# Kernel tuning notes

Hardware: AMD Instinct MI355X
Metric: run time of the kernel (lower is better)

Reference implementation:

```python
import jax, jax.numpy as jnp
import numpy as np

B, SEQ, DIM, HEADS = 2, 2048, 512, 8
HD = DIM // HEADS
RANK, DFF = 128, 1024
TAU_MEM, TAU_ADAPT, SLOPE, EPS = 0.99, 0.95, 25.0, 1e-6
THRESH, ADAPT_STRENGTH = 0.5, 0.1
TREE_LEVELS = int(np.log2(SEQ))  # 11


def rmsnorm(x, w, eps=EPS):
    return x * jax.lax.rsqrt(jnp.mean(x * x, axis=-1, keepdims=True) + eps) * w


def rope_cos_sin(seq, hd):
    inv = 1.0 / (10000.0 ** (jnp.arange(0, hd, 2, dtype=jnp.float32) / hd))
    f = jnp.arange(seq, dtype=jnp.float32)[:, None] * inv[None, :]  # [S, hd/2]
    emb = jnp.concatenate([f, f], axis=-1)  # [S, hd]
    return jnp.cos(emb), jnp.sin(emb)


def apply_rope(x, cos, sin):
    # x: [B, H, S, hd]; rotate-half formulation
    x1, x2 = jnp.split(x, 2, axis=-1)
    return x * cos + jnp.concatenate([-x2, x1], axis=-1) * sin


def setup_inputs() -> dict:
    key = jax.random.key(0)
    ks = jax.random.split(key, 12)
    w = lambda k, shape, fan: (jax.random.normal(k, shape, jnp.float32) / np.sqrt(fan))
    return {
        "x": jax.random.normal(ks[0], (B, SEQ, DIM), jnp.float32),
        "norm_w": jnp.ones((DIM,), jnp.float32),
        "wq": w(ks[1], (DIM, DIM), DIM),
        "wk": w(ks[2], (DIM, DIM), DIM),
        "wv": w(ks[3], (DIM, DIM), DIM),
        "wo": w(ks[4], (DIM, DIM), DIM),
        "lat_w": w(ks[5], (SEQ, SEQ), SEQ),
        "bt": jnp.full((DIM,), THRESH, jnp.float32),
        "as_w": jnp.full((DIM,), ADAPT_STRENGTH, jnp.float32),
        "gate_w": w(ks[6], (DIM, DIM), DIM),
        "tnorm1_w": jnp.ones((DIM,), jnp.float32),
        "tnorm2_w": jnp.ones((DIM,), jnp.float32),
        "ffn_norm_w": jnp.ones((DIM,), jnp.float32),
        "u_w": w(ks[7], (DIM, RANK), DIM),
        "v_w": w(ks[8], (RANK, 2 * DFF), RANK),
        "down_w": w(ks[9], (DFF, DIM), DFF),
    }


def reference(x, norm_w, wq, wk, wv, wo, lat_w, bt, as_w, gate_w,
              tnorm1_w, tnorm2_w, ffn_norm_w, u_w, v_w, down_w):
    Bx, S, D = x.shape
    # --- pre-norm + QKV projections (base_proj) ---
    h = rmsnorm(x, norm_w)
    q = (h @ wq.T).reshape(Bx, S, HEADS, HD).transpose(0, 2, 1, 3)  # [B,H,S,hd]
    k = (h @ wk.T).reshape(Bx, S, HEADS, HD).transpose(0, 2, 1, 3)
    v = (h @ wv.T).reshape(Bx, S, HEADS, HD).transpose(0, 2, 1, 3)
    # --- RoPE ---
    cos, sin = rope_cos_sin(S, HD)
    q = apply_rope(q, cos, sin)
    k = apply_rope(k, cos, sin)
    # --- causal self-attention ---
    scores = jnp.einsum("bhqd,bhkd->bhqk", q, k) / np.sqrt(HD)
    causal = jnp.tril(jnp.ones((S, S), bool))
    scores = jnp.where(causal, scores, jnp.float32(-1e9))
    attn = jnp.einsum("bhqk,bhkd->bhqd", jax.nn.softmax(scores, axis=-1), v)
    attn = attn.transpose(0, 2, 1, 3).reshape(Bx, S, D) @ wo.T
    # --- causal lateral mixing across sequence ---
    mixed = jnp.einsum("ts,bsd->btd", jnp.tril(lat_w), attn)
    # --- ALIF spiking recurrence over the sequence (soft surrogate spike) ---
    def alif_step(carry, i_t):
        vmem, ad = carry
        vmem = TAU_MEM * vmem + i_t
        th = bt + as_w * ad
        spike = jax.nn.sigmoid(SLOPE * (vmem - th))
        vmem = vmem - spike * th          # soft reset
        ad = TAU_ADAPT * ad + spike        # threshold adaptation
        return (vmem, ad), spike
    init = (jnp.zeros((Bx, D), x.dtype), jnp.zeros((Bx, D), x.dtype))
    _, spikes = jax.lax.scan(alif_step, init, mixed.transpose(1, 0, 2))
    spikes = spikes.transpose(1, 0, 2)  # [B,S,D]
    # --- fused addadd residual ---
    h2 = x + mixed + spikes
    # --- binary-tree cell recursion to a root summary ---
    s = h2
    for _ in range(TREE_LEVELS):
        raw = s[:, 0::2, :] + s[:, 1::2, :]         # pairwise sums (raw_sums)
        res = 0.5 * raw                              # residual / prev_s surrogate
        n = rmsnorm(raw, tnorm1_w)
        g = jax.nn.sigmoid(n @ gate_w.T)
        s = rmsnorm(g * n + (1.0 - g) * res, tnorm2_w)
    h3 = h2 + s[:, 0:1, :]  # broadcast root back over the sequence
    # --- low-rank SwiGLU FFN ---
    hn = rmsnorm(h3, ffn_norm_w)
    up = (hn @ u_w) @ v_w                 # [B,S,2*DFF]
    a, b = jnp.split(up, 2, axis=-1)
    ffn = (jax.nn.silu(a) * b) @ down_w   # [B,S,D]
    return h3 + ffn
```

## Files before the change

kernel.cpp:

```cpp
#include <hip/hip_runtime.h>
#include <math.h>

#define BB 2
#define SS 2048
#define DD 512
#define HH 8
#define HDD 64
#define RANKK 128
#define DFFF 1024

typedef short bf16x8 __attribute__((ext_vector_type(8)));
typedef float f32x4 __attribute__((ext_vector_type(4)));

__device__ __forceinline__ short f2b(float f) {
  union { float f; unsigned u; } v; v.f = f;
  unsigned r = v.u + 0x7FFF + ((v.u >> 16) & 1);
  return (short)(r >> 16);
}
__device__ __forceinline__ float b2f(short s) {
  union { unsigned u; float f; } v; v.u = ((unsigned)(unsigned short)s) << 16;
  return v.f;
}

__device__ __forceinline__ void gll16(const void* g, void* l) {
  __builtin_amdgcn_global_load_lds(
      (const __attribute__((address_space(1))) unsigned int*)g,
      (__attribute__((address_space(3))) unsigned int*)l, 16, 0, 0);
}

__device__ __forceinline__ float wsum(float v) {
#pragma unroll
  for (int off = 32; off > 0; off >>= 1) v += __shfl_xor(v, off, 64);
  return v;
}

__global__ void splitw4(const float* __restrict__ w0, const float* __restrict__ w1,
                        const float* __restrict__ w2, const float* __restrict__ w3,
                        short* h0, short* l0_, short* h1, short* l1_,
                        short* h2_, short* l2_, short* h3_, short* l3_) {
  const int z = blockIdx.z;
  const float* in = (z == 0) ? w0 : (z == 1) ? w1 : (z == 2) ? w2 : w3;
  short* hi = (z == 0) ? h0 : (z == 1) ? h1 : (z == 2) ? h2_ : h3_;
  short* lo = (z == 0) ? l0_ : (z == 1) ? l1_ : (z == 2) ? l2_ : l3_;
  int i = (blockIdx.x * 256 + threadIdx.x) * 4;
  if (i >= DD * DD) return;
  float4 v = *(const float4*)(in + i);
  short4 h4, l4;
  h4.x = f2b(v.x); l4.x = f2b(v.x - b2f(h4.x));
  h4.y = f2b(v.y); l4.y = f2b(v.y - b2f(h4.y));
  h4.z = f2b(v.z); l4.z = f2b(v.z - b2f(h4.z));
  h4.w = f2b(v.w); l4.w = f2b(v.w - b2f(h4.w));
  *(short4*)(hi + i) = h4;
  *(short4*)(lo + i) = l4;
}

__global__ void splitlat(const float* __restrict__ lat, short* __restrict__ hi,
                         short* __restrict__ lo) {
  int i = (blockIdx.x * 256 + threadIdx.x) * 4;
  int r = i >> 11;
  int c = i & 2047;
  float4 v = *(const float4*)(lat + i);
  if (c + 0 > r) v.x = 0.0f;
  if (c + 1 > r) v.y = 0.0f;
  if (c + 2 > r) v.z = 0.0f;
  if (c + 3 > r) v.w = 0.0f;
  short4 h4, l4;
  h4.x = f2b(v.x); l4.x = f2b(v.x - b2f(h4.x));
  h4.y = f2b(v.y); l4.y = f2b(v.y - b2f(h4.y));
  h4.z = f2b(v.z); l4.z = f2b(v.z - b2f(h4.z));
  h4.w = f2b(v.w); l4.w = f2b(v.w - b2f(h4.w));
  *(short4*)(hi + i) = h4;
  *(short4*)(lo + i) = l4;
}

__global__ void cvtb(const float* __restrict__ in, short* __restrict__ out, int n) {
  int i = (blockIdx.x * 256 + threadIdx.x) * 4;
  if (i >= n) return;
  float4 v = *(const float4*)(in + i);
  short4 o; o.x = f2b(v.x); o.y = f2b(v.y); o.z = f2b(v.z); o.w = f2b(v.w);
  *(short4*)(out + i) = o;
}

__global__ void sum2(const float* __restrict__ a, const float* __restrict__ bq,
                     float* __restrict__ o) {
  int i = (blockIdx.x * 256 + threadIdx.x) * 4;
  float4 va = *(const float4*)(a + i);
  float4 vb = *(const float4*)(bq + i);
  float4 vo = {va.x + vb.x, va.y + vb.y, va.z + vb.z, va.w + vb.w};
  *(float4*)(o + i) = vo;
}

__global__ void transp_cvt(const float* __restrict__ in, short* __restrict__ out,
                           int R, int C) {
  __shared__ float t[32][33];
  int c0 = blockIdx.x * 32, r0 = blockIdx.y * 32;
#pragma unroll
  for (int i = 0; i < 4; i++) {
    int idx = threadIdx.x + i * 256;
    int r = idx >> 5, c = idx & 31;
    t[r][c] = in[(size_t)(r0 + r) * C + c0 + c];
  }
  __syncthreads();
#pragma unroll
  for (int i = 0; i < 4; i++) {
    int idx = threadIdx.x + i * 256;
    int cc = idx >> 5, rr = idx & 31;
    out[(size_t)(c0 + cc) * R + r0 + rr] = f2b(t[rr][cc]);
  }
}

__global__ void rmsnorm_hl(const float* __restrict__ x, const float* __restrict__ w,
                           short* __restrict__ oh, short* __restrict__ ol, int rows) {
  int wid = blockIdx.x * 4 + (threadIdx.x >> 6);
  int lane = threadIdx.x & 63;
  if (wid >= rows) return;
  const float* xp = x + (size_t)wid * DD + lane * 8;
  float4 a = *(const float4*)xp;
  float4 b = *(const float4*)(xp + 4);
  float ss = a.x*a.x + a.y*a.y + a.z*a.z + a.w*a.w
           + b.x*b.x + b.y*b.y + b.z*b.z + b.w*b.w;
  ss = wsum(ss);
  float r = rsqrtf(ss * (1.0f / DD) + 1e-6f);
  const float* wp = w + lane * 8;
  float4 wa = *(const float4*)wp, wb = *(const float4*)(wp + 4);
  float o8[8] = {a.x*r*wa.x, a.y*r*wa.y, a.z*r*wa.z, a.w*r*wa.w,
                 b.x*r*wb.x, b.y*r*wb.y, b.z*r*wb.z, b.w*r*wb.w};
  short hv[8], lv[8];
#pragma unroll
  for (int i = 0; i < 8; i++) { hv[i] = f2b(o8[i]); lv[i] = f2b(o8[i] - b2f(hv[i])); }
  short* op = oh + (size_t)wid * DD + lane * 8;
  short* lp = ol + (size_t)wid * DD + lane * 8;
  *(short4*)op = make_short4(hv[0], hv[1], hv[2], hv[3]);
  *(short4*)(op + 4) = make_short4(hv[4], hv[5], hv[6], hv[7]);
  *(short4*)lp = make_short4(lv[0], lv[1], lv[2], lv[3]);
  *(short4*)(lp + 4) = make_short4(lv[4], lv[5], lv[6], lv[7]);
}

template <bool SPL, int OM, bool ROPE>
__global__ __launch_bounds__(256) void ggemm(const short* __restrict__ Ah_g,
                                             const short* __restrict__ Al_g,
                                             const short* __restrict__ Bh_g,
                                             const short* __restrict__ Bl_g,
                                             const float* __restrict__ ADD,
                                             void* __restrict__ C, void* __restrict__ C2,
                                             int M, int N, int K) {
  __shared__ short Ahs[128 * 32];
  __shared__ short Bhs[128 * 32];
  __shared__ short Als[SPL ? 128 * 32 : 8];
  __shared__ short Bls[SPL ? 128 * 32 : 8];
  const int tid = threadIdx.x, l = tid & 63, w = tid >> 6;
  const int wr = (w >> 1) * 64, wc = (w & 1) * 64;
  const int bm = blockIdx.y * 128, bn = blockIdx.x * 128;
  f32x4 acc[4][4] = {};
  for (int k0 = 0; k0 < K; k0 += 32) {
#pragma unroll
    for (int p = 0; p < 2; p++) {
      int row = p * 64 + (tid >> 2), g = tid & 3;
      int swz = (g ^ ((row >> 1) & 3)) * 8;
      gll16(Ah_g + (size_t)(bm + row) * K + k0 + swz, Ahs + p * 2048 + tid * 8);
      gll16(Bh_g + (size_t)(bn + row) * K + k0 + swz, Bhs + p * 2048 + tid * 8);
      if (SPL) {
        gll16(Al_g + (size_t)(bm + row) * K + k0 + swz, Als + p * 2048 + tid * 8);
        gll16(Bl_g + (size_t)(bn + row) * K + k0 + swz, Bls + p * 2048 + tid * 8);
      }
    }
    __syncthreads();
    bf16x8 ah[4], bh[4], al[4], bl[4];
#pragma unroll
    for (int m = 0; m < 4; m++) {
      int r = wr + m * 16 + (l & 15);
      int go = (((l >> 4) ^ ((r >> 1) & 3)) << 3);
      ah[m] = *(const bf16x8*)(Ahs + r * 32 + go);
      if (SPL) al[m] = *(const bf16x8*)(Als + r * 32 + go);
    }
#pragma unroll
    for (int n = 0; n < 4; n++) {
      int r = wc + n * 16 + (l & 15);
      int go = (((l >> 4) ^ ((r >> 1) & 3)) << 3);
      bh[n] = *(const bf16x8*)(Bhs + r * 32 + go);
      if (SPL) bl[n] = *(const bf16x8*)(Bls + r * 32 + go);
    }
#pragma unroll
    for (int m = 0; m < 4; m++)
#pragma unroll
      for (int n = 0; n < 4; n++) {
        acc[m][n] = __builtin_amdgcn_mfma_f32_16x16x32_bf16(ah[m], bh[n], acc[m][n], 0, 0, 0);
        if (SPL) {
          acc[m][n] = __builtin_amdgcn_mfma_f32_16x16x32_bf16(ah[m], bl[n], acc[m][n], 0, 0, 0);
          acc[m][n] = __builtin_amdgcn_mfma_f32_16x16x32_bf16(al[m], bh[n], acc[m][n], 0, 0, 0);
        }
      }
    __syncthreads();
  }
  const int ll = l & 15, lg4 = (l >> 4) * 4;
  if (ROPE) {
#pragma unroll
    for (int m = 0; m < 4; m++)
#pragma unroll
      for (int n = 0; n < 2; n++) {
        int i_ = n * 16 + ll;
        float inv = exp2f(-(float)i_ * (13.287712379549449f / 32.0f));
#pragma unroll
        for (int j = 0; j < 4; j++) {
          int gm = bm + wr + m * 16 + lg4 + j;
          int s = gm & (SS - 1);
          float ang = (float)s * inv;
          float sn, cs;
          sincosf(ang, &sn, &cs);
          float v1 = acc[m][n][j], v2 = acc[m][n + 2][j];
          acc[m][n][j]     = v1 * cs - v2 * sn;
          acc[m][n + 2][j] = v2 * cs + v1 * sn;
        }
      }
  }
#pragma unroll
  for (int m = 0; m < 4; m++)
#pragma unroll
    for (int n = 0; n < 4; n++) {
      int gn = bn + wc + n * 16 + ll;
#pragma unroll
      for (int j = 0; j < 4; j++) {
        int gm = bm + wr + m * 16 + lg4 + j;
        if (gm >= M || gn >= N) continue;
        float v = acc[m][n][j];
        if (OM == 0) {
          ((float*)C)[(size_t)gm * N + gn] = v;
        } else if (OM == 1) {
          ((short*)C)[(size_t)gm * N + gn] = f2b(v);
        } else if (OM == 6) {
          size_t off = (size_t)gm * N + gn;
          ((float*)C)[off] = v + ADD[off];
        } else {
          short hi = f2b(v);
          short lo = f2b(v - b2f(hi));
          int b = gm >> 11, s = gm & (SS - 1);
          int hh2 = gn >> 6, d = gn & 63;
          size_t off;
          if (OM == 2)      off = (((size_t)(b * HH + hh2)) * SS + s) * 64 + d;
          else if (OM == 3) off = (((size_t)(b * HH + hh2)) * 64 + d) * SS + s;
          else              off = ((size_t)(b * DD) + gn) * SS + s;
          ((short*)C)[off] = hi;
          ((short*)C2)[off] = lo;
        }
      }
    }
}

__global__ __launch_bounds__(256) void qkv_g(const short* __restrict__ Ah_g,
                                             const short* __restrict__ Al_g,
                                             const short* __restrict__ wh0, const short* __restrict__ wl0,
                                             const short* __restrict__ wh1, const short* __restrict__ wl1,
                                             const short* __restrict__ wh2, const short* __restrict__ wl2,
                                             short* __restrict__ c0h, short* __restrict__ c0l,
                                             short* __restrict__ c1h, short* __restrict__ c1l,
                                             short* __restrict__ c2h, short* __restrict__ c2l) {
  const int z = blockIdx.z;
  const short* Bh_g = (z == 0) ? wh0 : (z == 1) ? wh1 : wh2;
  const short* Bl_g = (z == 0) ? wl0 : (z == 1) ? wl1 : wl2;
  short* Ch = (z == 0) ? c0h : (z == 1) ? c1h : c2h;
  short* Cl = (z == 0) ? c0l : (z == 1) ? c1l : c2l;
  const int K = DD;
  __shared__ short Ahs[128 * 32];
  __shared__ short Bhs[128 * 32];
  __shared__ short Als[128 * 32];
  __shared__ short Bls[128 * 32];
  const int tid = threadIdx.x, l = tid & 63, w = tid >> 6;
  const int wr = (w >> 1) * 64, wc = (w & 1) * 64;
  const int bm = blockIdx.y * 128, bn = blockIdx.x * 128;
  f32x4 acc[4][4] = {};
  for (int k0 = 0; k0 < K; k0 += 32) {
#pragma unroll
    for (int p = 0; p < 2; p++) {
      int row = p * 64 + (tid >> 2), g = tid & 3;
      int swz = (g ^ ((row >> 1) & 3)) * 8;
      gll16(Ah_g + (size_t)(bm + row) * K + k0 + swz, Ahs + p * 2048 + tid * 8);
      gll16(Bh_g + (size_t)(bn + row) * K + k0 + swz, Bhs + p * 2048 + tid * 8);
      gll16(Al_g + (size_t)(bm + row) * K + k0 + swz, Als + p * 2048 + tid * 8);
      gll16(Bl_g + (size_t)(bn + row) * K + k0 + swz, Bls + p * 2048 + tid * 8);
    }
    __syncthreads();
    bf16x8 ah[4], bh[4], al[4], bl[4];
#pragma unroll
    for (int m = 0; m < 4; m++) {
      int r = wr + m * 16 + (l & 15);
      int go = (((l >> 4) ^ ((r >> 1) & 3)) << 3);
      ah[m] = *(const bf16x8*)(Ahs + r * 32 + go);
      al[m] = *(const bf16x8*)(Als + r * 32 + go);
    }
#pragma unroll
    for (int n = 0; n < 4; n++) {
      int r = wc + n * 16 + (l & 15);
      int go = (((l >> 4) ^ ((r >> 1) & 3)) << 3);
      bh[n] = *(const bf16x8*)(Bhs + r * 32 + go);
      bl[n] = *(const bf16x8*)(Bls + r * 32 + go);
    }
#pragma unroll
    for (int m = 0; m < 4; m++)
#pragma unroll
      for (int n = 0; n < 4; n++) {
        acc[m][n] = __builtin_amdgcn_mfma_f32_16x16x32_bf16(ah[m], bh[n], acc[m][n], 0, 0, 0);
        acc[m][n] = __builtin_amdgcn_mfma_f32_16x16x32_bf16(ah[m], bl[n], acc[m][n], 0, 0, 0);
        acc[m][n] = __builtin_amdgcn_mfma_f32_16x16x32_bf16(al[m], bh[n], acc[m][n], 0, 0, 0);
      }
    __syncthreads();
  }
  const int ll = l & 15, lg4 = (l >> 4) * 4;
  if (z < 2) {
#pragma unroll
    for (int m = 0; m < 4; m++)
#pragma unroll
      for (int n = 0; n < 2; n++) {
        int i_ = n * 16 + ll;
        float inv = exp2f(-(float)i_ * (13.287712379549449f / 32.0f));
#pragma unroll
        for (int j = 0; j < 4; j++) {
          int gm = bm + wr + m * 16 + lg4 + j;
          int s = gm & (SS - 1);
          float ang = (float)s * inv;
          float sn, cs;
          sincosf(ang, &sn, &cs);
          float v1 = acc[m][n][j], v2 = acc[m][n + 2][j];
          acc[m][n][j]     = v1 * cs - v2 * sn;
          acc[m][n + 2][j] = v2 * cs + v1 * sn;
        }
      }
  }
#pragma unroll
  for (int m = 0; m < 4; m++)
#pragma unroll
    for (int n = 0; n < 4; n++) {
      int gn = bn + wc + n * 16 + ll;
#pragma unroll
      for (int j = 0; j < 4; j++) {
        int gm = bm + wr + m * 16 + lg4 + j;
        float v = acc[m][n][j];
        short hi = f2b(v);
        short lo = f2b(v - b2f(hi));
        int b = gm >> 11, s = gm & (SS - 1);
        int hh2 = gn >> 6, d = gn & 63;
        size_t off = (z < 2) ? ((((size_t)(b * HH + hh2)) * SS + s) * 64 + d)
                             : ((((size_t)(b * HH + hh2)) * 64 + d) * SS + s);
        Ch[off] = hi;
        Cl[off] = lo;
      }
    }
}

__global__ __launch_bounds__(256) void lat_g(const short* __restrict__ lath,
                                             const short* __restrict__ latl,
                                             const short* __restrict__ bTh,
                                             const short* __restrict__ bTl,
                                             float* __restrict__ P0,
                                             float* __restrict__ P1) {
  const int zb = blockIdx.z >> 1;
  const int half = blockIdx.z & 1;
  bTh += (size_t)zb * DD * SS;
  bTl += (size_t)zb * DD * SS;
  float* Cc = (half == 0 ? P0 : P1) + (size_t)zb * DD * SS;
  __shared__ short Ah[128 * 32];
  __shared__ short Al[128 * 32];
  __shared__ short Bh[128 * 32];
  __shared__ short Bl[128 * 32];
  const int tid = threadIdx.x, l = tid & 63, w = tid >> 6;
  const int wr = (w >> 1) * 64, wc = (w & 1) * 64;
  const int bm = blockIdx.y * 128, bn = blockIdx.x * 128;
  const int T = blockIdx.y + 1;
  const int h0 = (T + 1) >> 1;
  const int kbeg = (half == 0) ? 0 : h0 * 128;
  const int kend = (half == 0) ? h0 * 128 : T * 128;
  f32x4 acc[4][4] = {};
  const int ll = l & 15, lg4 = (l >> 4) * 4;
  for (int k0 = kbeg; k0 < kend; k0 += 32) {
#pragma unroll
    for (int p = 0; p < 2; p++) {
      int row = p * 64 + (tid >> 2), g = tid & 3;
      int swz = (g ^ ((row >> 1) & 3)) * 8;
      gll16(bTh + (size_t)(bn + row) * SS + k0 + swz, Bh + p * 2048 + tid * 8);
      gll16(bTl + (size_t)(bn + row) * SS + k0 + swz, Bl + p * 2048 + tid * 8);
      gll16(lath + (size_t)(bm + row) * SS + k0 + swz, Ah + p * 2048 + tid * 8);
      gll16(latl + (size_t)(bm + row) * SS + k0 + swz, Al + p * 2048 + tid * 8);
    }
    __syncthreads();
    bf16x8 ah[4], bh[4], al[4], bl[4];
#pragma unroll
    for (int m = 0; m < 4; m++) {
      int r = wr + m * 16 + (l & 15);
      int go = (((l >> 4) ^ ((r >> 1) & 3)) << 3);
      ah[m] = *(const bf16x8*)(Ah + r * 32 + go);
      al[m] = *(const bf16x8*)(Al + r * 32 + go);
    }
#pragma unroll
    for (int n = 0; n < 4; n++) {
      int r = wc + n * 16 + (l & 15);
      int go = (((l >> 4) ^ ((r >> 1) & 3)) << 3);
      bh[n] = *(const bf16x8*)(Bh + r * 32 + go);
      bl[n] = *(const bf16x8*)(Bl + r * 32 + go);
    }
#pragma unroll
    for (int m = 0; m < 4; m++)
#pragma unroll
      for (int n = 0; n < 4; n++) {
        acc[m][n] = __builtin_amdgcn_mfma_f32_16x16x32_bf16(ah[m], bh[n], acc[m][n], 0, 0, 0);
        acc[m][n] = __builtin_amdgcn_mfma_f32_16x16x32_bf16(ah[m], bl[n], acc[m][n], 0, 0, 0);
        acc[m][n] = __builtin_amdgcn_mfma_f32_16x16x32_bf16(al[m], bh[n], acc[m][n], 0, 0, 0);
      }
    __syncthreads();
  }
#pragma unroll
  for (int m = 0; m < 4; m++)
#pragma unroll
    for (int n = 0; n < 4; n++) {
      int gn = bn + wc + n * 16 + ll;
#pragma unroll
      for (int j = 0; j < 4; j++) {
        int gm = bm + wr + m * 16 + lg4 + j;
        size_t off = ((size_t)((gm >> 5) * 512 + gn)) * 32 + ((gm + gn) & 31);
        Cc[off] = acc[m][n][j];
      }
    }
}

__global__ __launch_bounds__(256) void attn_g(const short* __restrict__ qh,
                                              const short* __restrict__ ql,
                                              const short* __restrict__ kh,
                                              const short* __restrict__ kl,
                                              const short* __restrict__ vh,
                                              const short* __restrict__ vl,
                                              short* __restrict__ aho,
                                              short* __restrict__ alo) {
  const int h = blockIdx.y, b = blockIdx.z;
  const int qt = (b == 0) ? (int)blockIdx.x : 31 - (int)blockIdx.x;
  const int q0 = qt * 64;
  const int tid = threadIdx.x, w = tid >> 6, l = tid & 63;
  const int lg = l >> 4, ll = l & 15;
  __shared__ short Kh[64 * 64], Kl[64 * 64];
  __shared__ short Vh[64 * 64], Vl[64 * 64];
  __shared__ short Ph[64 * 64];
  const size_t bh = (size_t)(b * HH + h);

  const int qr = q0 + w * 16 + ll;
  const short* qbh = qh + (bh * SS + qr) * 64;
  const short* qbl = ql + (bh * SS + qr) * 64;
  bf16x8 qfh[2], qfl[2];
#pragma unroll
  for (int ks = 0; ks < 2; ks++) {
    qfh[ks] = *(const bf16x8*)(qbh + (ks * 4 + lg) * 8);
    qfl[ks] = *(const bf16x8*)(qbl + (ks * 4 + lg) * 8);
  }

  f32x4 o[4] = {};
  float mrow[4] = {-1e30f, -1e30f, -1e30f, -1e30f};
  float lsum[4] = {};
  const int qrow0 = q0 + w * 16 + lg * 4;
  const int ntiles = qt + 1;

  for (int kt = 0; kt < ntiles; kt++) {
#pragma unroll
    for (int p = 0; p < 2; p++) {
      int row = p * 32 + (tid >> 3), g = tid & 7;
      int sw = ((g ^ (row & 7)) << 3);
      size_t krow = (bh * SS + kt * 64 + row) * 64;
      size_t vrow = (bh * 64 + row) * SS + kt * 64;
      gll16(kh + krow + sw, Kh + p * 2048 + tid * 8);
      gll16(kl + krow + sw, Kl + p * 2048 + tid * 8);
      gll16(vh + vrow + sw, Vh + p * 2048 + tid * 8);
      gll16(vl + vrow + sw, Vl + p * 2048 + tid * 8);
    }
    __syncthreads();

    f32x4 sv[4] = {};
#pragma unroll
    for (int nf = 0; nf < 4; nf++) {
      int r = nf * 16 + ll;
#pragma unroll
      for (int ks = 0; ks < 2; ks++) {
        int g = (ks * 4 + lg) ^ (r & 7);
        bf16x8 khf = *(const bf16x8*)(Kh + r * 64 + g * 8);
        bf16x8 klf = *(const bf16x8*)(Kl + r * 64 + g * 8);
        sv[nf] = __builtin_amdgcn_mfma_f32_16x16x32_bf16(qfh[ks], khf, sv[nf], 0, 0, 0);
        sv[nf] = __builtin_amdgcn_mfma_f32_16x16x32_bf16(qfh[ks], klf, sv[nf], 0, 0, 0);
        sv[nf] = __builtin_amdgcn_mfma_f32_16x16x32_bf16(qfl[ks], khf, sv[nf], 0, 0, 0);
      }
    }
#pragma unroll
    for (int nf = 0; nf < 4; nf++) {
      int kpos = kt * 64 + nf * 16 + ll;
#pragma unroll
      for (int j = 0; j < 4; j++) {
        float v = sv[nf][j] * 0.125f;
        sv[nf][j] = (kpos > qrow0 + j) ? -1e30f : v;
      }
    }
    float cf[4];
#pragma unroll
    for (int j = 0; j < 4; j++) {
      float r = fmaxf(fmaxf(sv[0][j], sv[1][j]), fmaxf(sv[2][j], sv[3][j]));
      r = fmaxf(r, __shfl_xor(r, 1)); r = fmaxf(r, __shfl_xor(r, 2));
      r = fmaxf(r, __shfl_xor(r, 4)); r = fmaxf(r, __shfl_xor(r, 8));
      float mn = fmaxf(mrow[j], r);
      cf[j] = __expf(mrow[j] - mn);
      mrow[j] = mn;
    }
    float ps[4] = {};
#pragma unroll
    for (int nf = 0; nf < 4; nf++)
#pragma unroll
      for (int j = 0; j < 4; j++) {
        float p = __expf(sv[nf][j] - mrow[j]);
        sv[nf][j] = p;
        ps[j] += p;
      }
#pragma unroll
    for (int j = 0; j < 4; j++) {
      float r = ps[j];
      r += __shfl_xor(r, 1); r += __shfl_xor(r, 2);
      r += __shfl_xor(r, 4); r += __shfl_xor(r, 8);
      lsum[j] = lsum[j] * cf[j] + r;
    }
#pragma unroll
    for (int nf = 0; nf < 4; nf++)
#pragma unroll
      for (int j = 0; j < 4; j++) o[nf][j] *= cf[j];
#pragma unroll
    for (int nf = 0; nf < 4; nf++)
#pragma unroll
      for (int j = 0; j < 4; j++) {
        int rowP = w * 16 + lg * 4 + j;
        int col = nf * 16 + ll;
        int off = rowP * 64 + (((col >> 3) ^ (rowP & 7)) << 3) + (col & 7);
        Ph[off] = f2b(sv[nf][j]);
      }
    __syncthreads();
    bf16x8 pfh[2];
    {
      int rowA = w * 16 + ll;
#pragma unroll
      for (int ks = 0; ks < 2; ks++) {
        int g = (ks * 4 + lg) ^ (rowA & 7);
        pfh[ks] = *(const bf16x8*)(Ph + rowA * 64 + g * 8);
      }
    }
#pragma unroll
    for (int nf = 0; nf < 4; nf++) {
      int r = nf * 16 + ll;
#pragma unroll
      for (int ks = 0; ks < 2; ks++) {
        int g = (ks * 4 + lg) ^ (r & 7);
        bf16x8 vhf = *(const bf16x8*)(Vh + r * 64 + g * 8);
        bf16x8 vlf = *(const bf16x8*)(Vl + r * 64 + g * 8);
        o[nf] = __builtin_amdgcn_mfma_f32_16x16x32_bf16(pfh[ks], vhf, o[nf], 0, 0, 0);
        o[nf] = __builtin_amdgcn_mfma_f32_16x16x32_bf16(pfh[ks], vlf, o[nf], 0, 0, 0);
      }
    }
    __syncthreads();
  }
  float inv[4];
#pragma unroll
  for (int j = 0; j < 4; j++) inv[j] = 1.0f / lsum[j];
#pragma unroll
  for (int nf = 0; nf < 4; nf++)
#pragma unroll
    for (int j = 0; j < 4; j++) {
      float v = o[nf][j] * inv[j];
      short hi = f2b(v);
      size_t off = ((size_t)(b * SS + qrow0 + j)) * DD + h * HDD + nf * 16 + ll;
      aho[off] = hi;
      alo[off] = f2b(v - b2f(hi));
    }
}

#define ACH 32
__global__ __launch_bounds__(64) void tsa_alif8(const float* __restrict__ mixedS,
                                                const float* __restrict__ bt,
                                                const float* __restrict__ asw,
                                                float* __restrict__ spikesS) {
  __shared__ float lds[2][ACH * 64];
  const int t = threadIdx.x;
  const int tid = blockIdx.x * 64 + t;
  const int b = tid >> 9, d = tid & 511;
  const int d0 = d & ~63;
  const float btd = bt[d], asd = asw[d];
  const float C = 36.06737602222409f;
  const float bt36 = btd * C, as36 = asd * C;
  const float bt99 = 0.99f * btd, as99 = 0.99f * asd;
  const size_t bbase = (size_t)b * DD * SS;
  const float* mp = mixedS + bbase;
  float* sp = spikesS + bbase;
  {
    const float* g0 = mp + (size_t)d0 * 32;
#pragma unroll
    for (int i = 0; i < 8; i++) gll16(g0 + i * 256 + t * 4, &lds[0][i * 256 + t * 4]);
  }
  float vR = 0.0f, ad = 0.0f;
  for (int c = 0; c < SS / ACH; c++) {
    const int cur = c & 1;
    __syncthreads();
    if (c + 1 < SS / ACH) {
      const float* gq = mp + ((size_t)((c + 1) * 512 + d0)) * 32;
#pragma unroll
      for (int i = 0; i < 8; i++) gll16(gq + i * 256 + t * 4, &lds[cur ^ 1][i * 256 + t * 4]);
    }
    float m[ACH];
#pragma unroll
    for (int j = 0; j < ACH; j++) m[j] = lds[cur][t * 32 + ((j + t) & 31)];
    vR += m[0];
    float sO[ACH];
#pragma unroll
    for (int j = 0; j < ACH; j++) {
      float thC = fmaf(ad, as36, bt36);
      float th99 = fmaf(ad, as99, bt99);
      float arg = fmaf(vR, -C, thC);
      float e = exp2f(arg);
      float s = __builtin_amdgcn_rcpf(1.0f + e);
      sO[j] = s;
      float pre = (j + 1 < ACH) ? fmaf(0.99f, vR, m[j + 1]) : (0.99f * vR);
      vR = fmaf(-th99, s, pre);
      ad = fmaf(0.95f, ad, s);
    }
#pragma unroll
    for (int j = 0; j < ACH; j++) lds[cur][t * 32 + ((j + t) & 31)] = sO[j];
    __syncthreads();
    float* so = sp + ((size_t)(c * 512 + d0)) * 32;
#pragma unroll
    for (int i = 0; i < 8; i++) {
      float4 v4 = *(const float4*)&lds[cur][i * 256 + t * 4];
      *(float4*)(so + i * 256 + t * 4) = v4;
    }
  }
}

__global__ __launch_bounds__(256) void fuse_h2(const float* __restrict__ x,
                                               const float* __restrict__ mixedS,
                                               const float* __restrict__ spikesS,
                                               float* __restrict__ h2) {
  const int s0 = blockIdx.x * 64, d0 = blockIdx.y * 64, b = blockIdx.z;
  __shared__ float t[64][65];
  const int dl = threadIdx.x >> 2;
  const int grp = threadIdx.x & 3;
  const size_t bbase = (size_t)b * DD * SS;
#pragma unroll
  for (int i = 0; i < 16; i++) {
    int sl = grp * 16 + i;
    int sg = s0 + sl;
    size_t off = bbase + ((size_t)((sg >> 5) * 512 + d0 + dl)) * 32 + ((sg + dl) & 31);
    t[dl][sl] = mixedS[off] + spikesS[off];
  }
  __syncthreads();
#pragma unroll
  for (int k = 0; k < 4; k++) {
    int sl = threadIdx.x >> 2;
    int dl2 = (threadIdx.x & 3) * 16 + k * 4;
    size_t off = ((size_t)(b * SS + s0 + sl)) * DD + d0 + dl2;
    float4 xv = *(const float4*)(x + off);
    float4 o;
    o.x = xv.x + t[dl2 + 0][sl];
    o.y = xv.y + t[dl2 + 1][sl];
    o.z = xv.z + t[dl2 + 2][sl];
    o.w = xv.w + t[dl2 + 3][sl];
    *(float4*)(h2 + off) = o;
  }
}

__global__ void tree_reduce_b(const float* __restrict__ sin_, const float* __restrict__ tn1,
                              short* __restrict__ nb, int Sn) {
  int wid = blockIdx.x * 4 + (threadIdx.x >> 6);
  int lane = threadIdx.x & 63;
  int rows = BB * Sn;
  if (wid >= rows) return;
  int b = wid / Sn, j = wid - b * Sn;
  const float* r0 = sin_ + ((size_t)(b * 2 * Sn + 2 * j)) * DD + lane * 8;
  const float* r1 = r0 + DD;
  float4 a0 = *(const float4*)r0, a1 = *(const float4*)(r0 + 4);
  float4 b0 = *(const float4*)r1, b1 = *(const float4*)(r1 + 4);
  float ra[8] = {a0.x + b0.x, a0.y + b0.y, a0.z + b0.z, a0.w + b0.w,
                 a1.x + b1.x, a1.y + b1.y, a1.z + b1.z, a1.w + b1.w};
  float ss = 0.0f;
#pragma unroll
  for (int i = 0; i < 8; i++) ss += ra[i] * ra[i];
  ss = wsum(ss);
  float rms = rsqrtf(ss * (1.0f / DD) + 1e-6f);
  const float* wp = tn1 + lane * 8;
  float4 wa = *(const float4*)wp, wb = *(const float4*)(wp + 4);
  float wv8[8] = {wa.x, wa.y, wa.z, wa.w, wb.x, wb.y, wb.z, wb.w};
  short* np = nb + (size_t)wid * DD + lane * 8;
  short4 n0, n1;
  n0.x = f2b(ra[0]*rms*wv8[0]); n0.y = f2b(ra[1]*rms*wv8[1]);
  n0.z = f2b(ra[2]*rms*wv8[2]); n0.w = f2b(ra[3]*rms*wv8[3]);
  n1.x = f2b(ra[4]*rms*wv8[4]); n1.y = f2b(ra[5]*rms*wv8[5]);
  n1.z = f2b(ra[6]*rms*wv8[6]); n1.w = f2b(ra[7]*rms*wv8[7]);
  *(short4*)np = n0;
  *(short4*)(np + 4) = n1;
}

__global__ void tree_combine_b(const float* __restrict__ g, const short* __restrict__ nb,
                               const float* __restrict__ sin_, const float* __restrict__ tn2,
                               float* __restrict__ sout, int Sn) {
  int wid = blockIdx.x * 4 + (threadIdx.x >> 6);
  int lane = threadIdx.x & 63;
  int rows = BB * Sn;
  if (wid >= rows) return;
  int b = wid / Sn, j = wid - b * Sn;
  const float* r0 = sin_ + ((size_t)(b * 2 * Sn + 2 * j)) * DD + lane * 8;
  const float* r1 = r0 + DD;
  float4 a0 = *(const float4*)r0, a1 = *(const float4*)(r0 + 4);
  float4 b0 = *(const float4*)r1, b1 = *(const float4*)(r1 + 4);
  float res[8] = {0.5f*(a0.x + b0.x), 0.5f*(a0.y + b0.y), 0.5f*(a0.z + b0.z), 0.5f*(a0.w + b0.w),
                  0.5f*(a1.x + b1.x), 0.5f*(a1.y + b1.y), 0.5f*(a1.z + b1.z), 0.5f*(a1.w + b1.w)};
  size_t base = (size_t)wid * DD + lane * 8;
  float t[8];
  float ss = 0.0f;
#pragma unroll
  for (int i = 0; i < 8; i++) {
    float gg = 1.0f / (1.0f + expf(-g[base + i]));
    float tv = gg * b2f(nb[base + i]) + (1.0f - gg) * res[i];
    t[i] = tv;
    ss += tv * tv;
  }
  ss = wsum(ss);
  float rms = rsqrtf(ss * (1.0f / DD) + 1e-6f);
#pragma unroll
  for (int i = 0; i < 8; i++) sout[base + i] = t[i] * rms * tn2[lane * 8 + i];
}

__global__ void h3hn_b(const float* __restrict__ h2, const float* __restrict__ root,
                       const float* __restrict__ fw, float* __restrict__ h3,
                       short* __restrict__ hn) {
  int wid = blockIdx.x * 4 + (threadIdx.x >> 6);
  int lane = threadIdx.x & 63;
  int b = wid >> 11;
  size_t base = (size_t)wid * DD + lane * 8;
  const float* rp = root + (size_t)b * DD + lane * 8;
  float t[8];
  float ss = 0.0f;
#pragma unroll
  for (int i = 0; i < 8; i++) {
    float tv = h2[base + i] + rp[i];
    t[i] = tv;
    ss += tv * tv;
    h3[base + i] = tv;
  }
  ss = wsum(ss);
  float rms = rsqrtf(ss * (1.0f / DD) + 1e-6f);
#pragma unroll
  for (int i = 0; i < 8; i++) hn[base + i] = f2b(t[i] * rms * fw[lane * 8 + i]);
}

__global__ __launch_bounds__(256) void upgate_g(const short* __restrict__ A,
                                                const short* __restrict__ Bv,
                                                short* __restrict__ ffa) {
  __shared__ short Ahs[128 * 32];
  __shared__ short B1s[128 * 32];
  __shared__ short B2s[128 * 32];
  const int tid = threadIdx.x, l = tid & 63, w = tid >> 6;
  const int wr = (w >> 1) * 64, wc = (w & 1) * 64;
  const int bm = blockIdx.y * 128, bn = blockIdx.x * 128;
  f32x4 acc1[4][4] = {}, acc2[4][4] = {};
  for (int k0 = 0; k0 < RANKK; k0 += 32) {
#pragma unroll
    for (int p = 0; p < 2; p++) {
      int row = p * 64 + (tid >> 2), g = tid & 3;
      int swz = (g ^ ((row >> 1) & 3)) * 8;
      gll16(A + (size_t)(bm + row) * RANKK + k0 + swz, Ahs + p * 2048 + tid * 8);
      gll16(Bv + (size_t)(bn + row) * RANKK + k0 + swz, B1s + p * 2048 + tid * 8);
      gll16(Bv + (size_t)(DFFF + bn + row) * RANKK + k0 + swz, B2s + p * 2048 + tid * 8);
    }
    __syncthreads();
    bf16x8 ah[4], b1[4], b2[4];
#pragma unroll
    for (int m = 0; m < 4; m++) {
      int r = wr + m * 16 + (l & 15);
      int go = (((l >> 4) ^ ((r >> 1) & 3)) << 3);
      ah[m] = *(const bf16x8*)(Ahs + r * 32 + go);
    }
#pragma unroll
    for (int n = 0; n < 4; n++) {
      int r = wc + n * 16 + (l & 15);
      int go = (((l >> 4) ^ ((r >> 1) & 3)) << 3);
      b1[n] = *(const bf16x8*)(B1s + r * 32 + go);
      b2[n] = *(const bf16x8*)(B2s + r * 32 + go);
    }
#pragma unroll
    for (int m = 0; m < 4; m++)
#pragma unroll
      for (int n = 0; n < 4; n++) {
        acc1[m][n] = __builtin_amdgcn_mfma_f32_16x16x32_bf16(ah[m], b1[n], acc1[m][n], 0, 0, 0);
        acc2[m][n] = __builtin_amdgcn_mfma_f32_16x16x32_bf16(ah[m], b2[n], acc2[m][n], 0, 0, 0);
      }
    __syncthreads();
  }
#pragma unroll
  for (int m = 0; m < 4; m++)
#pragma unroll
    for (int n = 0; n < 4; n++) {
      int gn = bn + wc + n * 16 + (l & 15);
#pragma unroll
      for (int j = 0; j < 4; j++) {
        int gm = bm + wr + m * 16 + (l >> 4) * 4 + j;
        float a = acc1[m][n][j];
        float s = a / (1.0f + __expf(-a));
        ffa[(size_t)gm * DFFF + gn] = f2b(s * acc2[m][n][j]);
      }
    }
}

extern "C" void kernel_launch(void* const* d_in, const int* in_sizes, int n_in,
                              void* d_out, int out_size, void* d_ws, size_t ws_size,
                              hipStream_t stream) {
  const float* x   = (const float*)d_in[0];
  const float* nw  = (const float*)d_in[1];
  const float* wq  = (const float*)d_in[2];
  const float* wk  = (const float*)d_in[3];
  const float* wv  = (const float*)d_in[4];
  const float* wo  = (const float*)d_in[5];
  const float* lat = (const float*)d_in[6];
  const float* btp = (const float*)d_in[7];
  const float* asw = (const float*)d_in[8];
  const float* gw  = (const float*)d_in[9];
  const float* tn1 = (const float*)d_in[10];
  const float* tn2 = (const float*)d_in[11];
  const float* fnw = (const float*)d_in[12];
  const float* uw  = (const float*)d_in[13];
  const float* vw  = (const float*)d_in[14];
  const float* dw  = (const float*)d_in[15];
  float* out = (float*)d_out;
  char* W = (char*)d_ws;
  const size_t MB = 1u << 20;

  short* h_hi = (short*)(W);
  short* h_lo = (short*)(W + 4 * MB);
  short* attn_hi = h_hi;
  short* attn_lo = h_lo;
  float* latP0 = (float*)(W);
  short* nb = (short*)(W);
  float* gb = (float*)(W + 2 * MB);
  short* q_hi = (short*)(W + 8 * MB);
  short* q_lo = (short*)(W + 12 * MB);
  short* apT_hi = q_hi;
  short* apT_lo = q_lo;
  float* spikesS = (float*)(W + 8 * MB);
  float* s0 = (float*)(W + 8 * MB);
  float* s1 = (float*)(W + 12 * MB);
  short* k_hi = (short*)(W + 16 * MB);
  short* k_lo = (short*)(W + 20 * MB);
  short* lath = (short*)(W + 16 * MB);
  short* hn = (short*)(W + 16 * MB);
  short* t1 = (short*)(W + 20 * MB);
  short* v_hi = (short*)(W + 24 * MB);
  short* v_lo = (short*)(W + 28 * MB);
  short* latl = (short*)(W + 24 * MB);
  float* h2 = (float*)(W + 24 * MB);
  short* ffa = (short*)(W + 24 * MB);
  float* latP1 = (float*)(W + 32 * MB);
  short* gwb = (short*)(W + 32 * MB);
  short* uwT = gwb + 262144;
  short* vwT = uwT + 65536;
  short* dwT = vwT + 262144;

  short* wqh = (short*)out;
  short* wql = wqh + 262144;
  short* wkh = wql + 262144;
  short* wkl = wkh + 262144;
  short* wvh = wkl + 262144;
  short* wvl = wvh + 262144;
  short* woh = wvl + 262144;
  short* wol = woh + 262144;

  const int rows = BB * SS;

  splitw4<<<dim3(256, 1, 4), 256, 0, stream>>>(wq, wk, wv, wo,
                                               wqh, wql, wkh, wkl, wvh, wvl, woh, wol);

  rmsnorm_hl<<<rows / 4, 256, 0, stream>>>(x, nw, h_hi, h_lo, rows);

  qkv_g<<<dim3(4, 32, 3), 256, 0, stream>>>(h_hi, h_lo,
                                            wqh, wql, wkh, wkl, wvh, wvl,
                                            q_hi, q_lo, k_hi, k_lo, v_hi, v_lo);

  attn_g<<<dim3(32, HH, BB), 256, 0, stream>>>(q_hi, q_lo, k_hi, k_lo, v_hi, v_lo,
                                               attn_hi, attn_lo);

  ggemm<true, 4, false><<<dim3(4, 32), 256, 0, stream>>>(
      attn_hi, attn_lo, woh, wol, nullptr, apT_hi, apT_lo, rows, DD, DD);

  splitlat<<<4096, 256, 0, stream>>>(lat, lath, latl);

  lat_g<<<dim3(4, 16, 4), 256, 0, stream>>>(lath, latl, apT_hi, apT_lo, latP0, latP1);

  sum2<<<(BB * DD * SS / 4) / 256, 256, 0, stream>>>(latP0, latP1, latP0);

  tsa_alif8<<<16, 64, 0, stream>>>(latP0, btp, asw, spikesS);
  fuse_h2<<<dim3(32, 8, 2), 256, 0, stream>>>(x, latP0, spikesS, h2);

  cvtb<<<256, 256, 0, stream>>>(gw, gwb, DD * DD);
  transp_cvt<<<dim3(4, 16), 256, 0, stream>>>(uw, uwT, DD, RANKK);
  transp_cvt<<<dim3(64, 4), 256, 0, stream>>>(vw, vwT, RANKK, 2 * DFFF);
  transp_cvt<<<dim3(16, 32), 256, 0, stream>>>(dw, dwT, DFFF, DD);

  const float* sin_ = h2;
  for (int lvl = 0; lvl < 11; lvl++) {
    int Sn = 1024 >> lvl;
    int r2 = BB * Sn;
    float* sout = (lvl & 1) ? s1 : s0;
    tree_reduce_b<<<(r2 + 3) / 4, 256, 0, stream>>>(sin_, tn1, nb, Sn);
    ggemm<false, 0, false><<<dim3(4, (r2 + 127) / 128), 256, 0, stream>>>(
        nb, nullptr, gwb, nullptr, nullptr, gb, nullptr, r2, DD, DD);
    tree_combine_b<<<(r2 + 3) / 4, 256, 0, stream>>>(gb, nb, sin_, tn2, sout, Sn);
    sin_ = sout;
  }

  h3hn_b<<<rows / 4, 256, 0, stream>>>(h2, sin_, fnw, out, hn);

  ggemm<false, 1, false><<<dim3(1, 32), 256, 0, stream>>>(
      hn, nullptr, uwT, nullptr, nullptr, t1, nullptr, rows, RANKK, DD);
  upgate_g<<<dim3(8, 32), 256, 0, stream>>>(t1, vwT, ffa);
  ggemm<false, 6, false><<<dim3(4, 32), 256, 0, stream>>>(
      ffa, nullptr, dwT, nullptr, out, out, nullptr, rows, DD, DFFF);
}
```

Measured before the change: 668.7 us.

## Fuse tree-level reduce, gate GEMM and combine into one kernel

Each tree level used to launch three kernels: pairwise sum plus rmsnorm, a gate GEMM, and sigmoid-gated combine plus rmsnorm. These are now one kernel per level. It computes the normalized pair sums on the fly into double-buffered LDS, runs a bf16 MFMA GEMM against the full gate weight, and applies the sigmoid blend and second rmsnorm in the epilogue. This removes 22 kernel launches and the nb/gb intermediate round trips. In exchange, each 32-row block streams all of gate_w, and deep levels with few rows run on very few blocks.

New measurement: 740.5 us. 1.11x slower.

```diff
diff --git a/kernel.cpp b/kernel.cpp
--- a/kernel.cpp
+++ b/kernel.cpp
@@ -661,65 +661,157 @@
   }
 }
 
-__global__ void tree_reduce_b(const float* __restrict__ sin_, const float* __restrict__ tn1,
-                              short* __restrict__ nb, int Sn) {
-  int wid = blockIdx.x * 4 + (threadIdx.x >> 6);
-  int lane = threadIdx.x & 63;
-  int rows = BB * Sn;
-  if (wid >= rows) return;
-  int b = wid / Sn, j = wid - b * Sn;
-  const float* r0 = sin_ + ((size_t)(b * 2 * Sn + 2 * j)) * DD + lane * 8;
-  const float* r1 = r0 + DD;
-  float4 a0 = *(const float4*)r0, a1 = *(const float4*)(r0 + 4);
-  float4 b0 = *(const float4*)r1, b1 = *(const float4*)(r1 + 4);
-  float ra[8] = {a0.x + b0.x, a0.y + b0.y, a0.z + b0.z, a0.w + b0.w,
-                 a1.x + b1.x, a1.y + b1.y, a1.z + b1.z, a1.w + b1.w};
-  float ss = 0.0f;
-#pragma unroll
-  for (int i = 0; i < 8; i++) ss += ra[i] * ra[i];
-  ss = wsum(ss);
-  float rms = rsqrtf(ss * (1.0f / DD) + 1e-6f);
-  const float* wp = tn1 + lane * 8;
-  float4 wa = *(const float4*)wp, wb = *(const float4*)(wp + 4);
-  float wv8[8] = {wa.x, wa.y, wa.z, wa.w, wb.x, wb.y, wb.z, wb.w};
-  short* np = nb + (size_t)wid * DD + lane * 8;
-  short4 n0, n1;
-  n0.x = f2b(ra[0]*rms*wv8[0]); n0.y = f2b(ra[1]*rms*wv8[1]);
-  n0.z = f2b(ra[2]*rms*wv8[2]); n0.w = f2b(ra[3]*rms*wv8[3]);
-  n1.x = f2b(ra[4]*rms*wv8[4]); n1.y = f2b(ra[5]*rms*wv8[5]);
-  n1.z = f2b(ra[6]*rms*wv8[6]); n1.w = f2b(ra[7]*rms*wv8[7]);
-  *(short4*)np = n0;
-  *(short4*)(np + 4) = n1;
-}
-
-__global__ void tree_combine_b(const float* __restrict__ g, const short* __restrict__ nb,
-                               const float* __restrict__ sin_, const float* __restrict__ tn2,
-                               float* __restrict__ sout, int Sn) {
-  int wid = blockIdx.x * 4 + (threadIdx.x >> 6);
-  int lane = threadIdx.x & 63;
-  int rows = BB * Sn;
-  if (wid >= rows) return;
-  int b = wid / Sn, j = wid - b * Sn;
-  const float* r0 = sin_ + ((size_t)(b * 2 * Sn + 2 * j)) * DD + lane * 8;
-  const float* r1 = r0 + DD;
-  float4 a0 = *(const float4*)r0, a1 = *(const float4*)(r0 + 4);
-  float4 b0 = *(const float4*)r1, b1 = *(const float4*)(r1 + 4);
-  float res[8] = {0.5f*(a0.x + b0.x), 0.5f*(a0.y + b0.y), 0.5f*(a0.z + b0.z), 0.5f*(a0.w + b0.w),
-                  0.5f*(a1.x + b1.x), 0.5f*(a1.y + b1.y), 0.5f*(a1.z + b1.z), 0.5f*(a1.w + b1.w)};
-  size_t base = (size_t)wid * DD + lane * 8;
-  float t[8];
-  float ss = 0.0f;
-#pragma unroll
-  for (int i = 0; i < 8; i++) {
-    float gg = 1.0f / (1.0f + expf(-g[base + i]));
-    float tv = gg * b2f(nb[base + i]) + (1.0f - gg) * res[i];
-    t[i] = tv;
-    ss += tv * tv;
-  }
-  ss = wsum(ss);
-  float rms = rsqrtf(ss * (1.0f / DD) + 1e-6f);
-#pragma unroll
-  for (int i = 0; i < 8; i++) sout[base + i] = t[i] * rms * tn2[lane * 8 + i];
+#define TRB 32
+__global__ __launch_bounds__(256) void tree_lvl(const float* __restrict__ pin,
+                                                const short* __restrict__ gwb,
+                                                const float* __restrict__ tn1,
+                                                const float* __restrict__ tn2,
+                                                float* __restrict__ sout, int R) {
+  __shared__ short Bs[2][512 * 32];
+  __shared__ short As[2][TRB * 32];
+  __shared__ float rms1[TRB];
+  __shared__ float rowpart[4][TRB];
+  __shared__ float rms2s[TRB];
+  const int tid = threadIdx.x, l = tid & 63, w = tid >> 6;
+  const int ll = l & 15, lg = l >> 4, lg4 = lg * 4;
+  const int bm = blockIdx.x * TRB;
+
+#pragma unroll
+  for (int it = 0; it < TRB / 4; it++) {
+    int row = it * 4 + w;
+    int gr = min(bm + row, R - 1);
+    const float* p0 = pin + (size_t)(2 * gr) * 512 + l * 8;
+    const float* p1 = p0 + 512;
+    float ss = 0.f;
+#pragma unroll
+    for (int e = 0; e < 8; e++) {
+      float rawv = p0[e] + p1[e];
+      ss += rawv * rawv;
+    }
+    ss = wsum(ss);
+    if (l == 0) rms1[row] = rsqrtf(ss * (1.0f / 512.0f) + 1e-6f);
+  }
+  __syncthreads();
+
+  f32x4 acc[2][8] = {};
+  {
+    int k0 = 0;
+#pragma unroll
+    for (int p = 0; p < 8; p++) {
+      int row = p * 64 + (tid >> 2), g = tid & 3;
+      int swz = (g ^ ((row >> 1) & 3)) * 8;
+      gll16(gwb + (size_t)row * 512 + k0 + swz, &Bs[0][row * 32 + g * 8]);
+    }
+    int row = tid >> 3, f4 = tid & 7;
+    int gr = min(bm + row, R - 1);
+    int kk = k0 + f4 * 4;
+    const float* p0 = pin + (size_t)(2 * gr) * 512 + kk;
+    const float* p1 = p0 + 512;
+    float r1v = rms1[row];
+    short4 hv;
+    hv.x = f2b((p0[0] + p1[0]) * r1v * tn1[kk + 0]);
+    hv.y = f2b((p0[1] + p1[1]) * r1v * tn1[kk + 1]);
+    hv.z = f2b((p0[2] + p1[2]) * r1v * tn1[kk + 2]);
+    hv.w = f2b((p0[3] + p1[3]) * r1v * tn1[kk + 3]);
+    int off = row * 32 + (((f4 >> 1) ^ ((row >> 1) & 3)) << 3) + (f4 & 1) * 4;
+    *(short4*)&As[0][off] = hv;
+  }
+  for (int kt = 0; kt < 16; kt++) {
+    int cur = kt & 1;
+    __syncthreads();
+    if (kt < 15) {
+      int k0 = (kt + 1) * 32;
+#pragma unroll
+      for (int p = 0; p < 8; p++) {
+        int row = p * 64 + (tid >> 2), g = tid & 3;
+        int swz = (g ^ ((row >> 1) & 3)) * 8;
+        gll16(gwb + (size_t)row * 512 + k0 + swz, &Bs[cur ^ 1][row * 32 + g * 8]);
+      }
+      int row = tid >> 3, f4 = tid & 7;
+      int gr = min(bm + row, R - 1);
+      int kk = k0 + f4 * 4;
+      const float* p0 = pin + (size_t)(2 * gr) * 512 + kk;
+      const float* p1 = p0 + 512;
+      float r1v = rms1[row];
+      short4 hv;
+      hv.x = f2b((p0[0] + p1[0]) * r1v * tn1[kk + 0]);
+      hv.y = f2b((p0[1] + p1[1]) * r1v * tn1[kk + 1]);
+      hv.z = f2b((p0[2] + p1[2]) * r1v * tn1[kk + 2]);
+      hv.w = f2b((p0[3] + p1[3]) * r1v * tn1[kk + 3]);
+      int off = row * 32 + (((f4 >> 1) ^ ((row >> 1) & 3)) << 3) + (f4 & 1) * 4;
+      *(short4*)&As[cur ^ 1][off] = hv;
+    }
+    bf16x8 af[2], bfg[8];
+#pragma unroll
+    for (int m = 0; m < 2; m++) {
+      int r = m * 16 + ll;
+      int go = ((lg ^ ((r >> 1) & 3)) << 3);
+      af[m] = *(const bf16x8*)&As[cur][r * 32 + go];
+    }
+#pragma unroll
+    for (int n = 0; n < 8; n++) {
+      int r = w * 128 + n * 16 + ll;
+      int go = ((lg ^ ((r >> 1) & 3)) << 3);
+      bfg[n] = *(const bf16x8*)&Bs[cur][r * 32 + go];
+    }
+#pragma unroll
+    for (int m = 0; m < 2; m++)
+#pragma unroll
+      for (int n = 0; n < 8; n++)
+        acc[m][n] = __builtin_amdgcn_mfma_f32_16x16x32_bf16(af[m], bfg[n], acc[m][n], 0, 0, 0);
+  }
+
+  float locsq[2][4] = {};
+#pragma unroll
+  for (int m = 0; m < 2; m++)
+#pragma unroll
+    for (int j = 0; j < 4; j++) {
+      int row = m * 16 + lg4 + j;
+      int gr = min(bm + row, R - 1);
+      float r1v = rms1[row];
+#pragma unroll
+      for (int n = 0; n < 8; n++) {
+        int col = w * 128 + n * 16 + ll;
+        float g = acc[m][n][j];
+        float sig = __builtin_amdgcn_rcpf(1.0f + __expf(-g));
+        float raw = pin[(size_t)(2 * gr) * 512 + col] + pin[(size_t)(2 * gr + 1) * 512 + col];
+        float nval = r1v * raw * tn1[col];
+        float res = 0.5f * raw;
+        float tv = sig * nval + (1.0f - sig) * res;
+        acc[m][n][j] = tv;
+        locsq[m][j] += tv * tv;
+      }
+    }
+#pragma unroll
+  for (int m = 0; m < 2; m++)
+#pragma unroll
+    for (int j = 0; j < 4; j++) {
+      float v = locsq[m][j];
+      v += __shfl_xor(v, 1); v += __shfl_xor(v, 2);
+      v += __shfl_xor(v, 4); v += __shfl_xor(v, 8);
+      if (ll == 0) rowpart[w][m * 16 + lg4 + j] = v;
+    }
+  __syncthreads();
+  if (tid < TRB) {
+    float s4 = rowpart[0][tid] + rowpart[1][tid] + rowpart[2][tid] + rowpart[3][tid];
+    rms2s[tid] = rsqrtf(s4 * (1.0f / 512.0f) + 1e-6f);
+  }
+  __syncthreads();
+#pragma unroll
+  for (int m = 0; m < 2; m++)
+#pragma unroll
+    for (int j = 0; j < 4; j++) {
+      int row = m * 16 + lg4 + j;
+      int gr = bm + row;
+      if (gr < R) {
+        float r2v = rms2s[row];
+#pragma unroll
+        for (int n = 0; n < 8; n++) {
+          int col = w * 128 + n * 16 + ll;
+          sout[(size_t)gr * 512 + col] = acc[m][n][j] * r2v * tn2[col];
+        }
+      }
+    }
 }
 
 __global__ void h3hn_b(const float* __restrict__ h2, const float* __restrict__ root,
@@ -831,8 +923,6 @@
   short* attn_hi = h_hi;
   short* attn_lo = h_lo;
   float* latP0 = (float*)(W);
-  short* nb = (short*)(W);
-  float* gb = (float*)(W + 2 * MB);
   short* q_hi = (short*)(W + 8 * MB);
   short* q_lo = (short*)(W + 12 * MB);
   short* apT_hi = q_hi;
@@ -898,14 +988,10 @@
 
   const float* sin_ = h2;
   for (int lvl = 0; lvl < 11; lvl++) {
-    int Sn = 1024 >> lvl;
-    int r2 = BB * Sn;
-    float* sout = (lvl & 1) ? s1 : s0;
-    tree_reduce_b<<<(r2 + 3) / 4, 256, 0, stream>>>(sin_, tn1, nb, Sn);
-    ggemm<false, 0, false><<<dim3(4, (r2 + 127) / 128), 256, 0, stream>>>(
-        nb, nullptr, gwb, nullptr, nullptr, gb, nullptr, r2, DD, DD);
-    tree_combine_b<<<(r2 + 3) / 4, 256, 0, stream>>>(gb, nb, sin_, tn2, sout, Sn);
-    sin_ = sout;
+    int R = BB * (1024 >> lvl);
+    float* sout_ = (lvl & 1) ? s1 : s0;
+    tree_lvl<<<dim3((R + TRB - 1) / TRB), 256, 0, stream>>>(sin_, gwb, tn1, tn2, sout_, R);
+    sin_ = sout_;
   }
 
   h3hn_b<<<rows / 4, 256, 0, stream>>>(h2, sin_, fnw, out, hn);
```
